# Performance work log

Hardware: AMD Instinct MI355X
Metric: run time of the kernel (lower is better)

## Reference

```python
import jax, jax.numpy as jnp
import numpy as np

N_NODES = 1_000_000
FEAT_DIM = 128
EMBED_DIM = 128
BATCH = 8192
NUM_SAMPLE = 10
N_LABELED = 16384
EPS = 1e-6
TEMP = 5.0


def setup_inputs() -> dict:
    key = jax.random.key(0)
    ks = jax.random.split(key, 8)
    return {
        "nodes": jax.random.randint(ks[0], (BATCH,), 0, N_NODES),
        "neigh_idx": jax.random.randint(ks[1], (BATCH, NUM_SAMPLE), 0, N_NODES),
        "pos_index": jax.random.randint(ks[2], (N_LABELED,), 0, N_NODES),
        "neg_index": jax.random.randint(ks[3], (N_LABELED,), 0, N_NODES),
        "features": jax.random.normal(ks[4], (N_NODES, FEAT_DIM), dtype=jnp.float32),
        "weight": jax.random.normal(ks[5], (EMBED_DIM, 2 * FEAT_DIM), dtype=jnp.float32) * (1.0 / np.sqrt(2 * FEAT_DIM)),
        "pos_vector": jax.random.normal(ks[6], (1, FEAT_DIM), dtype=jnp.float32),
        "neg_vector": jax.random.normal(ks[7], (1, FEAT_DIM), dtype=jnp.float32),
    }


def _update_vector(vec, x):
    # torch CosineSimilarity(dim=1, eps=1e-6) between [1,D] vec and [M,D] x -> [M]
    dot = jnp.einsum("md,d->m", x, vec[0])
    nv = jnp.maximum(jnp.linalg.norm(vec[0]), EPS)
    nx = jnp.maximum(jnp.linalg.norm(x, axis=1), EPS)
    cos = dot / (nv * nx)
    w = jax.nn.softmax(cos / TEMP)[None, :]  # softmax_with_temperature, t=5
    return jax.lax.stop_gradient(w @ x)  # [1, D], detached in torch


def reference(nodes, neigh_idx, pos_index, neg_index, features, weight, pos_vector, neg_vector):
    # Mean aggregator over sampled neighbors: [B, S, D] -> [B, D]
    neigh_feats = jnp.mean(features[neigh_idx], axis=1)
    # update_label_vector side computation (running vectors already initialized)
    new_pos = _update_vector(pos_vector, features[pos_index])
    new_neg = _update_vector(neg_vector, features[neg_index])
    # self features gather + concat + weight.mm + relu
    self_feats = features[nodes]                      # [B, D]
    combined = jnp.concatenate([self_feats, neigh_feats], axis=1)  # [B, 2D]
    out = jax.nn.relu(weight @ combined.T)            # [E, B]
    return out, new_pos, new_neg
```

## Files before the change

kernel.cpp:

```cpp
#include <hip/hip_runtime.h>
#include <hip/hip_bf16.h>
#include <stdint.h>

#define BATCH 8192
#define NSAMP 10
#define FDIM 128
#define K2 256
#define EDIM 128
#define NLAB 16384
#define EPSF 1e-6f

#define CPAD 264

typedef __bf16 bf16x8 __attribute__((ext_vector_type(8)));
typedef float f32x4 __attribute__((ext_vector_type(4)));

struct alignas(8) bfx4 { __hip_bfloat16 a, b, c, d; };

#define NPART 2048

__global__ __launch_bounds__(256) void fusedA(
    const int* __restrict__ nodes, const int* __restrict__ neigh,
    const int* __restrict__ pos_idx, const int* __restrict__ neg_idx,
    const float* __restrict__ feats,
    const float* __restrict__ pos_vec, const float* __restrict__ neg_vec,
    const float* __restrict__ W,
    float* __restrict__ partial,
    float* __restrict__ out)
{
    __shared__ __hip_bfloat16 comb[32][CPAD];

    int blk  = blockIdx.x;
    int tid  = threadIdx.x;
    int lane = tid & 63;
    int wv   = tid >> 6;
    int hl   = lane & 31;
    int half = lane >> 5;
    int hw   = wv * 2 + half;

    if (blk < 256) {
        int n0 = blk * 32;

        for (int rr = 0; rr < 4; ++rr) {
            int lr  = hw * 4 + rr;
            int row = n0 + lr;
            int ids[NSAMP + 1];
            ids[0] = nodes[row];
            #pragma unroll
            for (int j = 0; j < NSAMP; ++j) ids[1 + j] = neigh[row * NSAMP + j];

            f32x4 s = ((const f32x4*)(feats + (size_t)ids[0] * FDIM))[hl];
            f32x4 acc = {0.f, 0.f, 0.f, 0.f};
            #pragma unroll
            for (int j = 0; j < NSAMP; ++j) {
                f32x4 v = ((const f32x4*)(feats + (size_t)ids[1 + j] * FDIM))[hl];
                acc += v;
            }
            acc *= 0.1f;

            bfx4 t;
            t.a = __float2bfloat16(s[0]); t.b = __float2bfloat16(s[1]);
            t.c = __float2bfloat16(s[2]); t.d = __float2bfloat16(s[3]);
            *(bfx4*)(&comb[lr][4 * hl]) = t;
            t.a = __float2bfloat16(acc[0]); t.b = __float2bfloat16(acc[1]);
            t.c = __float2bfloat16(acc[2]); t.d = __float2bfloat16(acc[3]);
            *(bfx4*)(&comb[lr][FDIM + 4 * hl]) = t;
        }
        __syncthreads();

        int llo = lane & 15, lhi = lane >> 4;
        int m0 = wv * 32;

        f32x4 acc[2][2];
        #pragma unroll
        for (int i = 0; i < 2; ++i)
            #pragma unroll
            for (int j = 0; j < 2; ++j) { f32x4 z = {0.f,0.f,0.f,0.f}; acc[i][j] = z; }

        #pragma unroll
        for (int k0 = 0; k0 < K2; k0 += 32) {
            bf16x8 a[2], b[2];
            #pragma unroll
            for (int mi = 0; mi < 2; ++mi) {
                const float* wp = W + (size_t)(m0 + 16*mi + llo) * K2 + k0 + lhi*8;
                f32x4 w0 = ((const f32x4*)wp)[0];
                f32x4 w1 = ((const f32x4*)wp)[1];
                bf16x8 af;
                af[0] = (__bf16)w0[0]; af[1] = (__bf16)w0[1];
                af[2] = (__bf16)w0[2]; af[3] = (__bf16)w0[3];
                af[4] = (__bf16)w1[0]; af[5] = (__bf16)w1[1];
                af[6] = (__bf16)w1[2]; af[7] = (__bf16)w1[3];
                a[mi] = af;
            }
            #pragma unroll
            for (int ni = 0; ni < 2; ++ni) {
                const uint4* p = (const uint4*)(&comb[16*ni + llo][k0 + lhi*8]);
                b[ni] = __builtin_bit_cast(bf16x8, *p);
            }
            #pragma unroll
            for (int mi = 0; mi < 2; ++mi)
                #pragma unroll
                for (int ni = 0; ni < 2; ++ni)
                    acc[mi][ni] = __builtin_amdgcn_mfma_f32_16x16x32_bf16(a[mi], b[ni], acc[mi][ni], 0, 0, 0);
        }

        #pragma unroll
        for (int mi = 0; mi < 2; ++mi)
            #pragma unroll
            for (int ni = 0; ni < 2; ++ni)
                #pragma unroll
                for (int j = 0; j < 4; ++j) {
                    int row = m0 + 16*mi + lhi*4 + j;
                    int col = n0 + 16*ni + llo;
                    out[(size_t)row * BATCH + col] = fmaxf(acc[mi][ni][j], 0.f);
                }
    } else {
        int b     = blk - 256;
        int sel   = b >> 9;
        int inner = b & 511;
        int wid   = inner * 4 + wv;
        const int*   idx = sel ? neg_idx : pos_idx;
        const float* vec = sel ? neg_vec : pos_vec;

        f32x4 v4 = ((const f32x4*)vec)[hl];
        float pv = v4[0]*v4[0] + v4[1]*v4[1] + v4[2]*v4[2] + v4[3]*v4[3];
        #pragma unroll
        for (int off = 16; off; off >>= 1) pv += __shfl_xor(pv, off);
        float inv5nv = 1.f / (5.f * fmaxf(sqrtf(pv), EPSF));

        int base = wid * 8;
        int id[4];
        #pragma unroll
        for (int it = 0; it < 4; ++it) id[it] = idx[base + 2 * it + half];

        f32x4 x[4];
        #pragma unroll
        for (int it = 0; it < 4; ++it)
            x[it] = ((const f32x4*)(feats + (size_t)id[it] * FDIM))[hl];

        float d[4], nx[4];
        #pragma unroll
        for (int it = 0; it < 4; ++it) {
            d[it]  = x[it][0]*v4[0] + x[it][1]*v4[1] + x[it][2]*v4[2] + x[it][3]*v4[3];
            nx[it] = x[it][0]*x[it][0] + x[it][1]*x[it][1] + x[it][2]*x[it][2] + x[it][3]*x[it][3];
        }
        #pragma unroll
        for (int off = 16; off; off >>= 1) {
            #pragma unroll
            for (int it = 0; it < 4; ++it) {
                d[it]  += __shfl_xor(d[it], off);
                nx[it] += __shfl_xor(nx[it], off);
            }
        }

        f32x4 a4 = {0.f, 0.f, 0.f, 0.f};
        float es = 0.f;
        #pragma unroll
        for (int it = 0; it < 4; ++it) {
            float n2 = fmaxf(sqrtf(nx[it]), EPSF);
            float e = __expf(d[it] * inv5nv / n2);
            es += e;
            a4 += e * x[it];
        }

        #pragma unroll
        for (int c = 0; c < 4; ++c) a4[c] += __shfl_xor(a4[c], 32);
        es += __shfl_xor(es, 32);
        float* pw = partial + ((size_t)sel * NPART + wid) * 132;
        if (lane < 32) ((f32x4*)pw)[lane] = a4;
        if (lane == 0) pw[128] = es;
    }
}

__global__ __launch_bounds__(256) void stage2k(
    const float* __restrict__ partial, float* __restrict__ outv)
{
    int lane = threadIdx.x & 63;
    int wv   = threadIdx.x >> 6;
    int widx = blockIdx.x * 4 + wv;
    int sel = widx >> 7;
    int d   = widx & 127;
    const float* p = partial + (size_t)sel * NPART * 132;
    float s = 0.f, es = 0.f;
    for (int w = lane; w < NPART; w += 64) {
        s  += p[w * 132 + d];
        es += p[w * 132 + 128];
    }
    #pragma unroll
    for (int off = 32; off; off >>= 1) {
        s  += __shfl_xor(s, off);
        es += __shfl_xor(es, off);
    }
    if (lane == 0) outv[sel * 128 + d] = s / es;
}

extern "C" void kernel_launch(void* const* d_in, const int* in_sizes, int n_in,
                              void* d_out, int out_size, void* d_ws, size_t ws_size,
                              hipStream_t stream) {
    const int*   nodes = (const int*)d_in[0];
    const int*   neigh = (const int*)d_in[1];
    const int*   pos_i = (const int*)d_in[2];
    const int*   neg_i = (const int*)d_in[3];
    const float* feats = (const float*)d_in[4];
    const float* W     = (const float*)d_in[5];
    const float* pvec  = (const float*)d_in[6];
    const float* nvec  = (const float*)d_in[7];
    float* out = (float*)d_out;

    float* partial = (float*)d_ws;

    hipLaunchKernelGGL(fusedA, dim3(1280), dim3(256), 0, stream,
                       nodes, neigh, pos_i, neg_i, feats, pvec, nvec, W, partial, out);
    hipLaunchKernelGGL(stage2k, dim3(64), dim3(256), 0, stream,
                       partial, out + 1048576);
}
```

Before: 33.18 us.

## Merge GEMM and label-vector work into 256 blocks of 1024 threads

Cuts the grid from 1280 blocks of 256 threads to 256 blocks of 1024 threads. Each block gathers 32 rows with one row per half-wave, each wave computes a single 16x16 MFMA tile, and each wave then also does one label-vector partial. This removes the split between GEMM blocks and cosine-softmax blocks and raises gather parallelism per block. The cost is that only 256 large blocks run, so some CUs on a 256-CU part may get uneven work, and the heavy per-thread register use may limit occupancy at 1024 threads.

```diff
diff --git a/kernel.cpp b/kernel.cpp
--- a/kernel.cpp
+++ b/kernel.cpp
@@ -19,7 +19,7 @@
 
 #define NPART 2048
 
-__global__ __launch_bounds__(256) void fusedA(
+__global__ __launch_bounds__(1024) void fusedA(
     const int* __restrict__ nodes, const int* __restrict__ neigh,
     const int* __restrict__ pos_idx, const int* __restrict__ neg_idx,
     const float* __restrict__ feats,
@@ -38,87 +38,67 @@
     int half = lane >> 5;
     int hw   = wv * 2 + half;
 
-    if (blk < 256) {
-        int n0 = blk * 32;
+    int n0 = blk * 32;
 
-        for (int rr = 0; rr < 4; ++rr) {
-            int lr  = hw * 4 + rr;
-            int row = n0 + lr;
-            int ids[NSAMP + 1];
-            ids[0] = nodes[row];
-            #pragma unroll
-            for (int j = 0; j < NSAMP; ++j) ids[1 + j] = neigh[row * NSAMP + j];
+    {
+        int row = n0 + hw;
+        int ids[NSAMP + 1];
+        ids[0] = nodes[row];
+        #pragma unroll
+        for (int j = 0; j < NSAMP; ++j) ids[1 + j] = neigh[row * NSAMP + j];
 
-            f32x4 s = ((const f32x4*)(feats + (size_t)ids[0] * FDIM))[hl];
-            f32x4 acc = {0.f, 0.f, 0.f, 0.f};
-            #pragma unroll
-            for (int j = 0; j < NSAMP; ++j) {
-                f32x4 v = ((const f32x4*)(feats + (size_t)ids[1 + j] * FDIM))[hl];
-                acc += v;
-            }
-            acc *= 0.1f;
+        f32x4 s = ((const f32x4*)(feats + (size_t)ids[0] * FDIM))[hl];
+        f32x4 acc = {0.f, 0.f, 0.f, 0.f};
+        #pragma unroll
+        for (int j = 0; j < NSAMP; ++j) {
+            f32x4 v = ((const f32x4*)(feats + (size_t)ids[1 + j] * FDIM))[hl];
+            acc += v;
+        }
+        acc *= 0.1f;
 
-            bfx4 t;
-            t.a = __float2bfloat16(s[0]); t.b = __float2bfloat16(s[1]);
-            t.c = __float2bfloat16(s[2]); t.d = __float2bfloat16(s[3]);
-            *(bfx4*)(&comb[lr][4 * hl]) = t;
-            t.a = __float2bfloat16(acc[0]); t.b = __float2bfloat16(acc[1]);
-            t.c = __float2bfloat16(acc[2]); t.d = __float2bfloat16(acc[3]);
-            *(bfx4*)(&comb[lr][FDIM + 4 * hl]) = t;
-        }
-        __syncthreads();
+        bfx4 t;
+        t.a = __float2bfloat16(s[0]); t.b = __float2bfloat16(s[1]);
+        t.c = __float2bfloat16(s[2]); t.d = __float2bfloat16(s[3]);
+        *(bfx4*)(&comb[hw][4 * hl]) = t;
+        t.a = __float2bfloat16(acc[0]); t.b = __float2bfloat16(acc[1]);
+        t.c = __float2bfloat16(acc[2]); t.d = __float2bfloat16(acc[3]);
+        *(bfx4*)(&comb[hw][FDIM + 4 * hl]) = t;
+    }
+    __syncthreads();
 
+    {
         int llo = lane & 15, lhi = lane >> 4;
-        int m0 = wv * 32;
+        int mrow = (wv & 7) * 16;
+        int cgc  = (wv >> 3) * 16;
 
-        f32x4 acc[2][2];
-        #pragma unroll
-        for (int i = 0; i < 2; ++i)
-            #pragma unroll
-            for (int j = 0; j < 2; ++j) { f32x4 z = {0.f,0.f,0.f,0.f}; acc[i][j] = z; }
+        f32x4 cacc = {0.f, 0.f, 0.f, 0.f};
 
         #pragma unroll
         for (int k0 = 0; k0 < K2; k0 += 32) {
-            bf16x8 a[2], b[2];
-            #pragma unroll
-            for (int mi = 0; mi < 2; ++mi) {
-                const float* wp = W + (size_t)(m0 + 16*mi + llo) * K2 + k0 + lhi*8;
-                f32x4 w0 = ((const f32x4*)wp)[0];
-                f32x4 w1 = ((const f32x4*)wp)[1];
-                bf16x8 af;
-                af[0] = (__bf16)w0[0]; af[1] = (__bf16)w0[1];
-                af[2] = (__bf16)w0[2]; af[3] = (__bf16)w0[3];
-                af[4] = (__bf16)w1[0]; af[5] = (__bf16)w1[1];
-                af[6] = (__bf16)w1[2]; af[7] = (__bf16)w1[3];
-                a[mi] = af;
-            }
-            #pragma unroll
-            for (int ni = 0; ni < 2; ++ni) {
-                const uint4* p = (const uint4*)(&comb[16*ni + llo][k0 + lhi*8]);
-                b[ni] = __builtin_bit_cast(bf16x8, *p);
-            }
-            #pragma unroll
-            for (int mi = 0; mi < 2; ++mi)
-                #pragma unroll
-                for (int ni = 0; ni < 2; ++ni)
-                    acc[mi][ni] = __builtin_amdgcn_mfma_f32_16x16x32_bf16(a[mi], b[ni], acc[mi][ni], 0, 0, 0);
+            const float* wp = W + (size_t)(mrow + llo) * K2 + k0 + lhi*8;
+            f32x4 w0 = ((const f32x4*)wp)[0];
+            f32x4 w1 = ((const f32x4*)wp)[1];
+            bf16x8 a;
+            a[0] = (__bf16)w0[0]; a[1] = (__bf16)w0[1];
+            a[2] = (__bf16)w0[2]; a[3] = (__bf16)w0[3];
+            a[4] = (__bf16)w1[0]; a[5] = (__bf16)w1[1];
+            a[6] = (__bf16)w1[2]; a[7] = (__bf16)w1[3];
+            bf16x8 b = __builtin_bit_cast(bf16x8, *(const uint4*)(&comb[cgc + llo][k0 + lhi*8]));
+            cacc = __builtin_amdgcn_mfma_f32_16x16x32_bf16(a, b, cacc, 0, 0, 0);
         }
 
         #pragma unroll
-        for (int mi = 0; mi < 2; ++mi)
-            #pragma unroll
-            for (int ni = 0; ni < 2; ++ni)
-                #pragma unroll
-                for (int j = 0; j < 4; ++j) {
-                    int row = m0 + 16*mi + lhi*4 + j;
-                    int col = n0 + 16*ni + llo;
-                    out[(size_t)row * BATCH + col] = fmaxf(acc[mi][ni][j], 0.f);
-                }
-    } else {
-        int b     = blk - 256;
-        int sel   = b >> 9;
-        int inner = b & 511;
-        int wid   = inner * 4 + wv;
+        for (int j = 0; j < 4; ++j) {
+            int row = mrow + lhi*4 + j;
+            int col = n0 + cgc + llo;
+            out[(size_t)row * BATCH + col] = fmaxf(cacc[j], 0.f);
+        }
+    }
+
+    {
+        int gw  = blk * 16 + wv;
+        int sel = gw >> 11;
+        int wid = gw & 2047;
         const int*   idx = sel ? neg_idx : pos_idx;
         const float* vec = sel ? neg_vec : pos_vec;
 
@@ -209,7 +189,7 @@
 
     float* partial = (float*)d_ws;
 
-    hipLaunchKernelGGL(fusedA, dim3(1280), dim3(256), 0, stream,
+    hipLaunchKernelGGL(fusedA, dim3(256), dim3(1024), 0, stream,
                        nodes, neigh, pos_i, neg_i, feats, pvec, nvec, W, partial, out);
     hipLaunchKernelGGL(stage2k, dim3(64), dim3(256), 0, stream,
                        partial, out + 1048576);
```

After: 36.27 us. 9.3% more time.
